# Kernel optimization log

Measured on AMD Instinct MI355X. Metric: run time of the kernel, lower is better.

Reference implementation:

```python
import jax, jax.numpy as jnp
import numpy as np

N_NODES = 100000
N_EDGES = 3200000
IN_DIM = 512
HID_DIM = 16
OUT_DIM = 64


def _gcn_layer(E, X, W, b, n_nodes):
    # Standard GCN layer (CatGNN GCNLayer_MPNN_2):
    # add self-loops, symmetric deg^-1/2 normalization, project, gather-scatter sum.
    src = jnp.concatenate([E[0], jnp.arange(n_nodes, dtype=E.dtype)])
    dst = jnp.concatenate([E[1], jnp.arange(n_nodes, dtype=E.dtype)])
    deg = jax.ops.segment_sum(jnp.ones_like(dst, dtype=X.dtype), dst, num_segments=n_nodes)
    dinv = jnp.where(deg > 0, jax.lax.rsqrt(deg), 0.0)  # deg^-1/2, safe
    h = X @ W  # [N, d_out] project BEFORE aggregation (cheaper gather)
    norm = dinv[src] * dinv[dst]  # [E+N]
    msg = h[src] * norm[:, None]  # gather + scale
    out = jax.ops.segment_sum(msg, dst, num_segments=n_nodes)  # scatter-sum
    return out + b


def setup_inputs() -> dict:
    key = jax.random.key(0)
    k1, k2, k3, k4, k5 = jax.random.split(key, 5)
    V = jnp.arange(N_NODES, dtype=jnp.int64)
    E = jax.random.randint(k1, (2, N_EDGES), 0, N_NODES, dtype=jnp.int64)
    X = jax.random.normal(k2, (N_NODES, IN_DIM), dtype=jnp.float32)
    # Glorot-style init for layer weights
    W1 = jax.random.normal(k3, (IN_DIM, HID_DIM), dtype=jnp.float32) / np.sqrt(IN_DIM)
    b1 = jnp.zeros((HID_DIM,), dtype=jnp.float32)
    W2 = jax.random.normal(k4, (HID_DIM, OUT_DIM), dtype=jnp.float32) / np.sqrt(HID_DIM)
    b2 = jnp.zeros((OUT_DIM,), dtype=jnp.float32)
    return {"V": V, "E": E, "X": X, "W1": W1, "b1": b1, "W2": W2, "b2": b2}


def reference(V, E, X, W1, b1, W2, b2):
    n_nodes = V.shape[0]
    H = jax.nn.relu(_gcn_layer(E, X, W1, b1, n_nodes))
    # dropout is identity in eval mode
    H = _gcn_layer(E, H, W2, b2, n_nodes)
    return H
```

## Files before the change

kernel.cpp:

```cpp
#include <hip/hip_runtime.h>

#define HID 16
#define ODIM 64
#define IDIM 512
#define BKB 8
#define BKS 256
#define PTILE 4096
#define MAXBE 12288

__global__ __launch_bounds__(256) void k_bhist(const int* __restrict__ dst,
                                               int* __restrict__ bcnt, int ne, int nbk) {
    __shared__ int h[512];
    for (int t = threadIdx.x; t < 512; t += 256) h[t] = 0;
    __syncthreads();
    int stride = gridDim.x * blockDim.x;
    for (int e = blockIdx.x * blockDim.x + threadIdx.x; e < ne; e += stride)
        atomicAdd(&h[dst[e] >> BKB], 1);
    __syncthreads();
    for (int t = threadIdx.x; t < nbk; t += 256)
        if (h[t]) atomicAdd(&bcnt[t], h[t]);
}

__global__ __launch_bounds__(512) void k_bscan(const int* __restrict__ bcnt,
                                               int* __restrict__ bbase,
                                               int* __restrict__ bcur, int nbk) {
    __shared__ int s[512];
    int t = threadIdx.x;
    int v = (t < nbk) ? bcnt[t] : 0;
    s[t] = v;
    __syncthreads();
    for (int off = 1; off < 512; off <<= 1) {
        int u = (t >= off) ? s[t - off] : 0;
        __syncthreads();
        s[t] += u;
        __syncthreads();
    }
    if (t < nbk) { int b = s[t] - v; bbase[t] = b; bcur[t] = b; }
}

__global__ __launch_bounds__(512) void k_part(const int* __restrict__ src,
                                              const int* __restrict__ dst,
                                              int* __restrict__ bcur,
                                              unsigned int* __restrict__ ebuf,
                                              int ne, int nbk) {
    __shared__ int h[512], sc[512], base[512], lcur[512];
    __shared__ unsigned int sval[PTILE];
    __shared__ int saddr[PTILE];
    int e0 = blockIdx.x * PTILE;
    int m = ne - e0; if (m > PTILE) m = PTILE;
    if (m <= 0) return;
    int t = threadIdx.x;
    h[t] = 0;
    __syncthreads();
    for (int k = t; k < m; k += 512) atomicAdd(&h[dst[e0 + k] >> BKB], 1);
    __syncthreads();
    int hv = h[t];
    sc[t] = hv;
    __syncthreads();
    for (int off = 1; off < 512; off <<= 1) {
        int u = (t >= off) ? sc[t - off] : 0;
        __syncthreads();
        sc[t] += u;
        __syncthreads();
    }
    base[t] = hv ? atomicAdd(&bcur[t], hv) : 0;
    lcur[t] = 0;
    __syncthreads();
    for (int k = t; k < m; k += 512) {
        int d = dst[e0 + k];
        int b = d >> BKB;
        int r = atomicAdd(&lcur[b], 1);
        int slot = sc[b] - h[b] + r;
        sval[slot] = ((unsigned int)src[e0 + k] << BKB) | (unsigned int)(d & (BKS - 1));
        saddr[slot] = base[b] + r;
    }
    __syncthreads();
    for (int k = t; k < m; k += 512) ebuf[saddr[k]] = sval[k];
}

__global__ __launch_bounds__(512) void k_csr(const int* __restrict__ bbase,
                                             const int* __restrict__ bcnt,
                                             const unsigned int* __restrict__ ebuf,
                                             int* __restrict__ cnt,
                                             int* __restrict__ row_start,
                                             int* __restrict__ csr_src, int n) {
    __shared__ int h[256], sc[256], lc[256];
    __shared__ int stage[MAXBE];
    int bk = blockIdx.x;
    int node0 = bk << BKB;
    int ebase = bbase[bk];
    int ecnt = bcnt[bk];
    int t = threadIdx.x;
    if (t < 256) { h[t] = 0; lc[t] = 0; }
    __syncthreads();
    for (int k = t; k < ecnt; k += 512) atomicAdd(&h[ebuf[ebase + k] & (BKS - 1)], 1);
    __syncthreads();
    int hv = (t < 256) ? h[t] : 0;
    if (t < 256) sc[t] = hv;
    __syncthreads();
    for (int off = 1; off < 256; off <<= 1) {
        int u = (t >= off && t < 256) ? sc[t - off] : 0;
        __syncthreads();
        if (t < 256) sc[t] += u;
        __syncthreads();
    }
    if (t < 256) {
        int node = node0 + t;
        if (node < n) { cnt[node] = hv; row_start[node] = ebase + sc[t] - hv; }
    }
    if (ecnt <= MAXBE) {
        for (int k = t; k < ecnt; k += 512) {
            unsigned int p = ebuf[ebase + k];
            int dl = p & (BKS - 1);
            int r = atomicAdd(&lc[dl], 1);
            stage[sc[dl] - h[dl] + r] = (int)(p >> BKB);
        }
        __syncthreads();
        for (int k = t; k < ecnt; k += 512) csr_src[ebase + k] = stage[k];
    } else {
        for (int k = t; k < ecnt; k += 512) {
            unsigned int p = ebuf[ebase + k];
            int dl = p & (BKS - 1);
            int r = atomicAdd(&lc[dl], 1);
            csr_src[ebase + sc[dl] - h[dl] + r] = (int)(p >> BKB);
        }
    }
}

__device__ __forceinline__ void fmaq(float4& a, float s, float4 w) {
    a.x = fmaf(s, w.x, a.x);
    a.y = fmaf(s, w.y, a.y);
    a.z = fmaf(s, w.z, a.z);
    a.w = fmaf(s, w.w, a.w);
}

__global__ __launch_bounds__(256) void k_proj1(const float* __restrict__ X,
                                               const float* __restrict__ W1,
                                               const int* __restrict__ cnt,
                                               float* __restrict__ hs1, int n) {
    int i = blockIdx.x * 256 + threadIdx.x;
    if (i >= n) return;

    const float4* __restrict__ xr = (const float4*)(X + (size_t)i * IDIM);
    const float4* __restrict__ W4 = (const float4*)W1;
    float4 a0 = make_float4(0.f, 0.f, 0.f, 0.f), a1 = a0, a2 = a0, a3 = a0;

    for (int k4 = 0; k4 < IDIM / 4; ++k4) {
        float4 x = xr[k4];
        const float4* w = W4 + k4 * 16;
        fmaq(a0, x.x, w[0]);  fmaq(a1, x.x, w[1]);  fmaq(a2, x.x, w[2]);  fmaq(a3, x.x, w[3]);
        fmaq(a0, x.y, w[4]);  fmaq(a1, x.y, w[5]);  fmaq(a2, x.y, w[6]);  fmaq(a3, x.y, w[7]);
        fmaq(a0, x.z, w[8]);  fmaq(a1, x.z, w[9]);  fmaq(a2, x.z, w[10]); fmaq(a3, x.z, w[11]);
        fmaq(a0, x.w, w[12]); fmaq(a1, x.w, w[13]); fmaq(a2, x.w, w[14]); fmaq(a3, x.w, w[15]);
    }

    float di = rsqrtf((float)(cnt[i] + 1));
    a0.x *= di; a0.y *= di; a0.z *= di; a0.w *= di;
    a1.x *= di; a1.y *= di; a1.z *= di; a1.w *= di;
    a2.x *= di; a2.y *= di; a2.z *= di; a2.w *= di;
    a3.x *= di; a3.y *= di; a3.z *= di; a3.w *= di;
    float4* h4 = (float4*)(hs1 + (size_t)i * HID);
    h4[0] = a0; h4[1] = a1; h4[2] = a2; h4[3] = a3;
}

__device__ __forceinline__ float4 gacc(int rs, int c, int q,
                                       const int* __restrict__ csr_src,
                                       const float4* __restrict__ h4,
                                       float4 acc) {
    int k = 0;
    int head = (-rs) & 3;
    if (head > c) head = c;
    for (; k < head; ++k) {
        float4 v = h4[(size_t)csr_src[rs + k] * 4 + q];
        acc.x += v.x; acc.y += v.y; acc.z += v.z; acc.w += v.w;
    }
    for (; k + 3 < c; k += 4) {
        int4 s = *(const int4*)(csr_src + rs + k);
        float4 v0 = h4[(size_t)s.x * 4 + q];
        float4 v1 = h4[(size_t)s.y * 4 + q];
        float4 v2 = h4[(size_t)s.z * 4 + q];
        float4 v3 = h4[(size_t)s.w * 4 + q];
        acc.x += v0.x; acc.y += v0.y; acc.z += v0.z; acc.w += v0.w;
        acc.x += v1.x; acc.y += v1.y; acc.z += v1.z; acc.w += v1.w;
        acc.x += v2.x; acc.y += v2.y; acc.z += v2.z; acc.w += v2.w;
        acc.x += v3.x; acc.y += v3.y; acc.z += v3.z; acc.w += v3.w;
    }
    for (; k < c; ++k) {
        float4 v = h4[(size_t)csr_src[rs + k] * 4 + q];
        acc.x += v.x; acc.y += v.y; acc.z += v.z; acc.w += v.w;
    }
    return acc;
}

__global__ __launch_bounds__(256) void k_gather_mid(const int* __restrict__ row_start,
                                                    const int* __restrict__ cnt,
                                                    const int* __restrict__ csr_src,
                                                    const float* __restrict__ hs,
                                                    const float* __restrict__ b1,
                                                    float* __restrict__ outbuf, int n) {
    int tid = blockIdx.x * blockDim.x + threadIdx.x;
    int i = tid >> 2;
    int q = tid & 3;
    if (i >= n) return;
    const float4* h4 = (const float4*)hs;
    int rs = row_start[i];
    int c = cnt[i];
    float4 acc = gacc(rs, c, q, csr_src, h4, h4[(size_t)i * 4 + q]);
    float di = rsqrtf((float)(c + 1));
    float4 b = ((const float4*)b1)[q];
    float4 r;
    r.x = fmaxf(fmaf(di, acc.x, b.x), 0.f) * di;
    r.y = fmaxf(fmaf(di, acc.y, b.y), 0.f) * di;
    r.z = fmaxf(fmaf(di, acc.z, b.z), 0.f) * di;
    r.w = fmaxf(fmaf(di, acc.w, b.w), 0.f) * di;
    ((float4*)outbuf)[(size_t)i * 4 + q] = r;
}

__global__ __launch_bounds__(256) void k_gather(const int* __restrict__ row_start,
                                                const int* __restrict__ cnt,
                                                const int* __restrict__ csr_src,
                                                const float* __restrict__ hs,
                                                float* __restrict__ agg, int n) {
    int tid = blockIdx.x * blockDim.x + threadIdx.x;
    int i = tid >> 2;
    int q = tid & 3;
    if (i >= n) return;
    const float4* h4 = (const float4*)hs;
    int rs = row_start[i];
    int c = cnt[i];
    float4 acc = gacc(rs, c, q, csr_src, h4, h4[(size_t)i * 4 + q]);
    ((float4*)agg)[(size_t)i * 4 + q] = acc;
}

__global__ __launch_bounds__(256) void k_out(const int* __restrict__ cnt,
                                             const float* __restrict__ agg2,
                                             const float* __restrict__ W2,
                                             const float* __restrict__ b2,
                                             float* __restrict__ out, int n) {
    __shared__ float Ws[HID * ODIM];
    __shared__ float bs[ODIM];
    int t = threadIdx.x;
    for (int u = t; u < HID * ODIM; u += 256) Ws[u] = W2[u];
    if (t < ODIM) bs[t] = b2[t];
    __syncthreads();

    int j = t & 63;
    int slot = t >> 6;
    int i0 = blockIdx.x * 16 + slot * 4;

    float wc[HID];
#pragma unroll
    for (int k = 0; k < HID; ++k) wc[k] = Ws[k * ODIM + j];
    float bj = bs[j];

    const float4* g4 = (const float4*)agg2;
#pragma unroll
    for (int u = 0; u < 4; ++u) {
        int i = i0 + u;
        if (i < n) {
            float4 g0 = g4[(size_t)i * 4 + 0];
            float4 g1 = g4[(size_t)i * 4 + 1];
            float4 g2 = g4[(size_t)i * 4 + 2];
            float4 g3 = g4[(size_t)i * 4 + 3];
            float acc = g0.x * wc[0]  + g0.y * wc[1]  + g0.z * wc[2]  + g0.w * wc[3]
                      + g1.x * wc[4]  + g1.y * wc[5]  + g1.z * wc[6]  + g1.w * wc[7]
                      + g2.x * wc[8]  + g2.y * wc[9]  + g2.z * wc[10] + g2.w * wc[11]
                      + g3.x * wc[12] + g3.y * wc[13] + g3.z * wc[14] + g3.w * wc[15];
            float di = rsqrtf((float)(cnt[i] + 1));
            out[(size_t)i * ODIM + j] = fmaf(di, acc, bj);
        }
    }
}

extern "C" void kernel_launch(void* const* d_in, const int* in_sizes, int n_in,
                              void* d_out, int out_size, void* d_ws, size_t ws_size,
                              hipStream_t stream) {
    const int* E = (const int*)d_in[1];
    const float* X = (const float*)d_in[2];
    const float* W1 = (const float*)d_in[3];
    const float* b1 = (const float*)d_in[4];
    const float* W2 = (const float*)d_in[5];
    const float* b2 = (const float*)d_in[6];
    float* out = (float*)d_out;

    const int n = in_sizes[0];
    const int ne = in_sizes[1] / 2;
    const int* src = E;
    const int* dst = E + ne;
    const int nbk = (n + BKS - 1) >> BKB;

    char* ws = (char*)d_ws;
    int* bcnt = (int*)ws;
    int* bbase = (int*)(ws + (8u << 10));
    int* bcur = (int*)(ws + (16u << 10));
    int* cnt = (int*)(ws + (1u << 20));
    int* row_start = (int*)(ws + (2u << 20));
    unsigned int* ebuf = (unsigned int*)(ws + (3u << 20));
    float* B1 = (float*)(ws + (3u << 20));
    float* B2 = (float*)(ws + (10u << 20));
    int* csr_src = (int*)(ws + (17u << 20));

    hipMemsetAsync(bcnt, 0, nbk * sizeof(int), stream);
    k_bhist<<<1024, 256, 0, stream>>>(dst, bcnt, ne, nbk);
    k_bscan<<<1, 512, 0, stream>>>(bcnt, bbase, bcur, nbk);
    k_part<<<(ne + PTILE - 1) / PTILE, 512, 0, stream>>>(src, dst, bcur, ebuf, ne, nbk);
    k_csr<<<nbk, 512, 0, stream>>>(bbase, bcnt, ebuf, cnt, row_start, csr_src, n);

    k_proj1<<<(n + 255) / 256, 256, 0, stream>>>(X, W1, cnt, B1, n);
    k_gather_mid<<<(n * 4 + 255) / 256, 256, 0, stream>>>(row_start, cnt, csr_src, B1, b1, B2, n);
    k_gather<<<(n * 4 + 255) / 256, 256, 0, stream>>>(row_start, cnt, csr_src, B2, B1, n);
    k_out<<<(n + 15) / 16, 256, 0, stream>>>(cnt, B1, W2, b2, out, n);
}
```

Before: 528.4 us.

## Replace bucketed two-pass CSR build with atomic histogram, scan and scatter

Swaps the bucket-partition CSR construction (block histogram, partition into an edge buffer, then a per-bucket local sort) for a direct per-node atomic histogram, a three-kernel prefix scan, and an atomic-cursor scatter of source indices. It also unrolls the projection loop and splits the gather accumulation across two accumulators with an 8-wide unrolled loop to expose more memory-level parallelism. The new CSR build drops one full pass over the edges and the intermediate buffer, but it relies on millions of global atomics and leaves neighbour order within each row nondeterministic, which can change the float summation order and scatter the writes.

Result: slower. 847.3 us (+60.4%).

```diff
diff --git a/kernel.cpp b/kernel.cpp
--- a/kernel.cpp
+++ b/kernel.cpp
@@ -3,30 +3,38 @@
 #define HID 16
 #define ODIM 64
 #define IDIM 512
-#define BKB 8
-#define BKS 256
-#define PTILE 4096
-#define MAXBE 12288
-
-__global__ __launch_bounds__(256) void k_bhist(const int* __restrict__ dst,
-                                               int* __restrict__ bcnt, int ne, int nbk) {
-    __shared__ int h[512];
-    for (int t = threadIdx.x; t < 512; t += 256) h[t] = 0;
-    __syncthreads();
+
+__global__ __launch_bounds__(256) void k_hist(const int* __restrict__ dst,
+                                              int* __restrict__ cnt, int ne) {
     int stride = gridDim.x * blockDim.x;
     for (int e = blockIdx.x * blockDim.x + threadIdx.x; e < ne; e += stride)
-        atomicAdd(&h[dst[e] >> BKB], 1);
+        atomicAdd(&cnt[dst[e]], 1);
+}
+
+__global__ __launch_bounds__(256) void k_scan1(const int* __restrict__ cnt,
+                                               int* __restrict__ row_start,
+                                               int* __restrict__ bsum, int n) {
+    __shared__ int s[256];
+    int t = threadIdx.x;
+    int node = blockIdx.x * 256 + t;
+    int c = (node < n) ? cnt[node] : 0;
+    s[t] = c;
     __syncthreads();
-    for (int t = threadIdx.x; t < nbk; t += 256)
-        if (h[t]) atomicAdd(&bcnt[t], h[t]);
-}
-
-__global__ __launch_bounds__(512) void k_bscan(const int* __restrict__ bcnt,
-                                               int* __restrict__ bbase,
-                                               int* __restrict__ bcur, int nbk) {
+    for (int off = 1; off < 256; off <<= 1) {
+        int u = (t >= off) ? s[t - off] : 0;
+        __syncthreads();
+        s[t] += u;
+        __syncthreads();
+    }
+    if (node < n) row_start[node] = s[t] - c;
+    if (t == 255) bsum[blockIdx.x] = s[255];
+}
+
+__global__ __launch_bounds__(512) void k_scan2(const int* __restrict__ bsum,
+                                               int* __restrict__ bbase, int nbk) {
     __shared__ int s[512];
     int t = threadIdx.x;
-    int v = (t < nbk) ? bcnt[t] : 0;
+    int v = (t < nbk) ? bsum[t] : 0;
     s[t] = v;
     __syncthreads();
     for (int off = 1; off < 512; off <<= 1) {
@@ -35,95 +43,29 @@
         s[t] += u;
         __syncthreads();
     }
-    if (t < nbk) { int b = s[t] - v; bbase[t] = b; bcur[t] = b; }
-}
-
-__global__ __launch_bounds__(512) void k_part(const int* __restrict__ src,
+    if (t < nbk) bbase[t] = s[t] - v;
+}
+
+__global__ __launch_bounds__(256) void k_scan3(int* __restrict__ row_start,
+                                               const int* __restrict__ bbase,
+                                               int* __restrict__ cur, int n) {
+    int node = blockIdx.x * 256 + threadIdx.x;
+    if (node < n) {
+        int r = row_start[node] + bbase[blockIdx.x];
+        row_start[node] = r;
+        cur[node] = r;
+    }
+}
+
+__global__ __launch_bounds__(256) void k_scat(const int* __restrict__ src,
                                               const int* __restrict__ dst,
-                                              int* __restrict__ bcur,
-                                              unsigned int* __restrict__ ebuf,
-                                              int ne, int nbk) {
-    __shared__ int h[512], sc[512], base[512], lcur[512];
-    __shared__ unsigned int sval[PTILE];
-    __shared__ int saddr[PTILE];
-    int e0 = blockIdx.x * PTILE;
-    int m = ne - e0; if (m > PTILE) m = PTILE;
-    if (m <= 0) return;
-    int t = threadIdx.x;
-    h[t] = 0;
-    __syncthreads();
-    for (int k = t; k < m; k += 512) atomicAdd(&h[dst[e0 + k] >> BKB], 1);
-    __syncthreads();
-    int hv = h[t];
-    sc[t] = hv;
-    __syncthreads();
-    for (int off = 1; off < 512; off <<= 1) {
-        int u = (t >= off) ? sc[t - off] : 0;
-        __syncthreads();
-        sc[t] += u;
-        __syncthreads();
-    }
-    base[t] = hv ? atomicAdd(&bcur[t], hv) : 0;
-    lcur[t] = 0;
-    __syncthreads();
-    for (int k = t; k < m; k += 512) {
-        int d = dst[e0 + k];
-        int b = d >> BKB;
-        int r = atomicAdd(&lcur[b], 1);
-        int slot = sc[b] - h[b] + r;
-        sval[slot] = ((unsigned int)src[e0 + k] << BKB) | (unsigned int)(d & (BKS - 1));
-        saddr[slot] = base[b] + r;
-    }
-    __syncthreads();
-    for (int k = t; k < m; k += 512) ebuf[saddr[k]] = sval[k];
-}
-
-__global__ __launch_bounds__(512) void k_csr(const int* __restrict__ bbase,
-                                             const int* __restrict__ bcnt,
-                                             const unsigned int* __restrict__ ebuf,
-                                             int* __restrict__ cnt,
-                                             int* __restrict__ row_start,
-                                             int* __restrict__ csr_src, int n) {
-    __shared__ int h[256], sc[256], lc[256];
-    __shared__ int stage[MAXBE];
-    int bk = blockIdx.x;
-    int node0 = bk << BKB;
-    int ebase = bbase[bk];
-    int ecnt = bcnt[bk];
-    int t = threadIdx.x;
-    if (t < 256) { h[t] = 0; lc[t] = 0; }
-    __syncthreads();
-    for (int k = t; k < ecnt; k += 512) atomicAdd(&h[ebuf[ebase + k] & (BKS - 1)], 1);
-    __syncthreads();
-    int hv = (t < 256) ? h[t] : 0;
-    if (t < 256) sc[t] = hv;
-    __syncthreads();
-    for (int off = 1; off < 256; off <<= 1) {
-        int u = (t >= off && t < 256) ? sc[t - off] : 0;
-        __syncthreads();
-        if (t < 256) sc[t] += u;
-        __syncthreads();
-    }
-    if (t < 256) {
-        int node = node0 + t;
-        if (node < n) { cnt[node] = hv; row_start[node] = ebase + sc[t] - hv; }
-    }
-    if (ecnt <= MAXBE) {
-        for (int k = t; k < ecnt; k += 512) {
-            unsigned int p = ebuf[ebase + k];
-            int dl = p & (BKS - 1);
-            int r = atomicAdd(&lc[dl], 1);
-            stage[sc[dl] - h[dl] + r] = (int)(p >> BKB);
-        }
-        __syncthreads();
-        for (int k = t; k < ecnt; k += 512) csr_src[ebase + k] = stage[k];
-    } else {
-        for (int k = t; k < ecnt; k += 512) {
-            unsigned int p = ebuf[ebase + k];
-            int dl = p & (BKS - 1);
-            int r = atomicAdd(&lc[dl], 1);
-            csr_src[ebase + sc[dl] - h[dl] + r] = (int)(p >> BKB);
-        }
+                                              int* __restrict__ cur,
+                                              int* __restrict__ csr_src, int ne) {
+    int stride = gridDim.x * blockDim.x;
+    for (int e = blockIdx.x * blockDim.x + threadIdx.x; e < ne; e += stride) {
+        int s = src[e];
+        int p = atomicAdd(&cur[dst[e]], 1);
+        csr_src[p] = s;
     }
 }
 
@@ -145,6 +87,7 @@
     const float4* __restrict__ W4 = (const float4*)W1;
     float4 a0 = make_float4(0.f, 0.f, 0.f, 0.f), a1 = a0, a2 = a0, a3 = a0;
 
+#pragma unroll 4
     for (int k4 = 0; k4 < IDIM / 4; ++k4) {
         float4 x = xr[k4];
         const float4* w = W4 + k4 * 16;
@@ -163,32 +106,46 @@
     h4[0] = a0; h4[1] = a1; h4[2] = a2; h4[3] = a3;
 }
 
+__device__ __forceinline__ void acc4(float4& a, float4 v) {
+    a.x += v.x; a.y += v.y; a.z += v.z; a.w += v.w;
+}
+
 __device__ __forceinline__ float4 gacc(int rs, int c, int q,
                                        const int* __restrict__ csr_src,
                                        const float4* __restrict__ h4,
                                        float4 acc) {
+    float4 acc2 = make_float4(0.f, 0.f, 0.f, 0.f);
     int k = 0;
     int head = (-rs) & 3;
     if (head > c) head = c;
-    for (; k < head; ++k) {
-        float4 v = h4[(size_t)csr_src[rs + k] * 4 + q];
-        acc.x += v.x; acc.y += v.y; acc.z += v.z; acc.w += v.w;
+    for (; k < head; ++k)
+        acc4(acc, h4[(size_t)csr_src[rs + k] * 4 + q]);
+    for (; k + 7 < c; k += 8) {
+        int4 s0 = *(const int4*)(csr_src + rs + k);
+        int4 s1 = *(const int4*)(csr_src + rs + k + 4);
+        float4 v0 = h4[(size_t)s0.x * 4 + q];
+        float4 v1 = h4[(size_t)s0.y * 4 + q];
+        float4 v2 = h4[(size_t)s0.z * 4 + q];
+        float4 v3 = h4[(size_t)s0.w * 4 + q];
+        float4 w0 = h4[(size_t)s1.x * 4 + q];
+        float4 w1 = h4[(size_t)s1.y * 4 + q];
+        float4 w2 = h4[(size_t)s1.z * 4 + q];
+        float4 w3 = h4[(size_t)s1.w * 4 + q];
+        acc4(acc, v0);  acc4(acc2, w0);
+        acc4(acc, v1);  acc4(acc2, w1);
+        acc4(acc, v2);  acc4(acc2, w2);
+        acc4(acc, v3);  acc4(acc2, w3);
     }
     for (; k + 3 < c; k += 4) {
         int4 s = *(const int4*)(csr_src + rs + k);
-        float4 v0 = h4[(size_t)s.x * 4 + q];
-        float4 v1 = h4[(size_t)s.y * 4 + q];
-        float4 v2 = h4[(size_t)s.z * 4 + q];
-        float4 v3 = h4[(size_t)s.w * 4 + q];
-        acc.x += v0.x; acc.y += v0.y; acc.z += v0.z; acc.w += v0.w;
-        acc.x += v1.x; acc.y += v1.y; acc.z += v1.z; acc.w += v1.w;
-        acc.x += v2.x; acc.y += v2.y; acc.z += v2.z; acc.w += v2.w;
-        acc.x += v3.x; acc.y += v3.y; acc.z += v3.z; acc.w += v3.w;
-    }
-    for (; k < c; ++k) {
-        float4 v = h4[(size_t)csr_src[rs + k] * 4 + q];
-        acc.x += v.x; acc.y += v.y; acc.z += v.z; acc.w += v.w;
-    }
+        acc4(acc, h4[(size_t)s.x * 4 + q]);
+        acc4(acc2, h4[(size_t)s.y * 4 + q]);
+        acc4(acc, h4[(size_t)s.z * 4 + q]);
+        acc4(acc2, h4[(size_t)s.w * 4 + q]);
+    }
+    for (; k < c; ++k)
+        acc4(acc, h4[(size_t)csr_src[rs + k] * 4 + q]);
+    acc4(acc, acc2);
     return acc;
 }
 
@@ -287,24 +244,24 @@
     const int ne = in_sizes[1] / 2;
     const int* src = E;
     const int* dst = E + ne;
-    const int nbk = (n + BKS - 1) >> BKB;
+    const int nbk = (n + 255) >> 8;
 
     char* ws = (char*)d_ws;
-    int* bcnt = (int*)ws;
+    int* bsum = (int*)ws;
     int* bbase = (int*)(ws + (8u << 10));
-    int* bcur = (int*)(ws + (16u << 10));
     int* cnt = (int*)(ws + (1u << 20));
     int* row_start = (int*)(ws + (2u << 20));
-    unsigned int* ebuf = (unsigned int*)(ws + (3u << 20));
+    int* cur = (int*)(ws + (2u << 20) + (512u << 10));
     float* B1 = (float*)(ws + (3u << 20));
     float* B2 = (float*)(ws + (10u << 20));
     int* csr_src = (int*)(ws + (17u << 20));
 
-    hipMemsetAsync(bcnt, 0, nbk * sizeof(int), stream);
-    k_bhist<<<1024, 256, 0, stream>>>(dst, bcnt, ne, nbk);
-    k_bscan<<<1, 512, 0, stream>>>(bcnt, bbase, bcur, nbk);
-    k_part<<<(ne + PTILE - 1) / PTILE, 512, 0, stream>>>(src, dst, bcur, ebuf, ne, nbk);
-    k_csr<<<nbk, 512, 0, stream>>>(bbase, bcnt, ebuf, cnt, row_start, csr_src, n);
+    hipMemsetAsync(cnt, 0, n * sizeof(int), stream);
+    k_hist<<<2048, 256, 0, stream>>>(dst, cnt, ne);
+    k_scan1<<<nbk, 256, 0, stream>>>(cnt, row_start, bsum, n);
+    k_scan2<<<1, 512, 0, stream>>>(bsum, bbase, nbk);
+    k_scan3<<<nbk, 256, 0, stream>>>(row_start, bbase, cur, n);
+    k_scat<<<2048, 256, 0, stream>>>(src, dst, cur, csr_src, ne);
 
     k_proj1<<<(n + 255) / 256, 256, 0, stream>>>(X, W1, cnt, B1, n);
     k_gather_mid<<<(n * 4 + 255) / 256, 256, 0, stream>>>(row_start, cnt, csr_src, B1, b1, B2, n);
```
